# Optimization experiments

Measured on AMD Instinct MI355X. Metric: run time of the kernel, lower is better.

Reference implementation:

```python
import jax, jax.numpy as jnp
import numpy as np

QMIN = 0.0
QMAX = 255.0  # uint8, asymmetric


def fake_quant(x, scale, zp):
    # asymmetric uint8 fake-quantization: q = clamp(round(x/s + zp), 0, 255); dq = (q - zp) * s
    s = scale.reshape(())
    z = zp.reshape(())
    q = jnp.clip(jnp.round(x / s + z), QMIN, QMAX)
    return (q - z) * s


def setup_inputs() -> dict:
    key = jax.random.key(0)
    k1, k2 = jax.random.split(key)
    B, M, K, N = 4, 2048, 4096, 4096
    x1 = jax.random.normal(k1, (B, M, K), dtype=jnp.float32)
    x2 = jax.random.normal(k2, (B, K, N), dtype=jnp.float32)
    # realistic learned per-tensor scale / zero-point for ~N(0,1) data over uint8 range
    x1_scale = jnp.full((1,), 8.0 / 255.0, dtype=jnp.float32)
    x1_zp = jnp.full((1,), 128.0, dtype=jnp.float32)
    x2_scale = jnp.full((1,), 8.0 / 255.0, dtype=jnp.float32)
    x2_zp = jnp.full((1,), 128.0, dtype=jnp.float32)
    return {"x1": x1, "x2": x2, "x1_scale": x1_scale, "x1_zp": x1_zp,
            "x2_scale": x2_scale, "x2_zp": x2_zp}


def reference(x1, x2, x1_scale, x1_zp, x2_scale, x2_zp):
    q1 = fake_quant(x1, x1_scale, x1_zp)  # [B, M, K]
    q2 = fake_quant(x2, x2_scale, x2_zp)  # [B, K, N]
    return jnp.matmul(q1, q2)             # [B, M, N]
```

## Files before the change

### kernel.cpp

```cpp
#include <hip/hip_runtime.h>
#include <stdint.h>

typedef int v4i __attribute__((ext_vector_type(4)));

#define GLOBAL_AS __attribute__((address_space(1)))
#define LDS_AS __attribute__((address_space(3)))

__device__ __forceinline__ int quant1(float x, float s, float z, int zi) {
    float q = rintf(x / s + z);
    q = fminf(fmaxf(q, 0.0f), 255.0f);
    return (int)q - zi;
}

__device__ __forceinline__ unsigned qpack4(float4 v, float s, float z, int zi) {
    unsigned q0 = (unsigned)(quant1(v.x, s, z, zi) & 255);
    unsigned q1 = (unsigned)(quant1(v.y, s, z, zi) & 255);
    unsigned q2 = (unsigned)(quant1(v.z, s, z, zi) & 255);
    unsigned q3 = (unsigned)(quant1(v.w, s, z, zi) & 255);
    return q0 | (q1 << 8) | (q2 << 16) | (q3 << 24);
}

__global__ __launch_bounds__(256) void quant_lin(const float* __restrict__ x,
                                                 int8_t* __restrict__ out,
                                                 const float* __restrict__ sp,
                                                 const float* __restrict__ zp,
                                                 long n16) {
    float s = sp[0], z = zp[0];
    int zi = (int)rintf(z);
    long i = (long)blockIdx.x * 256 + threadIdx.x;
    if (i >= n16) return;
    const float4* xv = (const float4*)x;
    uint4 w;
    w.x = qpack4(xv[i * 4 + 0], s, z, zi);
    w.y = qpack4(xv[i * 4 + 1], s, z, zi);
    w.z = qpack4(xv[i * 4 + 2], s, z, zi);
    w.w = qpack4(xv[i * 4 + 3], s, z, zi);
    ((uint4*)out)[i] = w;
}

__global__ __launch_bounds__(256) void quant_bt(const float* __restrict__ x,
                                                int8_t* __restrict__ out,
                                                const float* __restrict__ sp,
                                                const float* __restrict__ zp) {
    constexpr int K = 4096, N = 4096;
    float s = sp[0], z = zp[0];
    int zi = (int)rintf(z);
    size_t bin = (size_t)blockIdx.z * K * N;
    int tid = threadIdx.x;
    int bk = tid >> 4;
    int bn = tid & 15;
    int k0 = blockIdx.y * 64, n0 = blockIdx.x * 64;
    __shared__ unsigned lds[64][17];
    unsigned o0 = 0, o1 = 0, o2 = 0, o3 = 0;
#pragma unroll
    for (int r = 0; r < 4; ++r) {
        float4 v = *(const float4*)(x + bin + (size_t)(k0 + bk * 4 + r) * N + n0 + bn * 4);
        o0 |= (unsigned)(quant1(v.x, s, z, zi) & 255) << (r * 8);
        o1 |= (unsigned)(quant1(v.y, s, z, zi) & 255) << (r * 8);
        o2 |= (unsigned)(quant1(v.z, s, z, zi) & 255) << (r * 8);
        o3 |= (unsigned)(quant1(v.w, s, z, zi) & 255) << (r * 8);
    }
    lds[bn * 4 + 0][bk] = o0;
    lds[bn * 4 + 1][bk] = o1;
    lds[bn * 4 + 2][bk] = o2;
    lds[bn * 4 + 3][bk] = o3;
    __syncthreads();
    int nl = tid >> 2, ch = tid & 3;
    uint4 w;
    w.x = lds[nl][ch * 4 + 0];
    w.y = lds[nl][ch * 4 + 1];
    w.z = lds[nl][ch * 4 + 2];
    w.w = lds[nl][ch * 4 + 3];
    *(uint4*)(out + bin + (size_t)(n0 + nl) * K + k0 + ch * 16) = w;
}

__global__ __launch_bounds__(512, 2) void gemm_i8(const int8_t* __restrict__ A,
                                                  const int8_t* __restrict__ Bt,
                                                  float* __restrict__ C,
                                                  const float* __restrict__ sp1,
                                                  const float* __restrict__ sp2) {
    constexpr int M = 2048, N = 4096, K = 4096;
    constexpr int BM = 256, BN = 256, BK = 128;
    constexpr int NT = K / BK;
    constexpr int NBN = N / BN;

    extern __shared__ char smem[];

    int b = blockIdx.z;
    const int8_t* Ab = A + (size_t)b * M * K;
    const int8_t* Bb = Bt + (size_t)b * N * K;
    float* Cb = C + (size_t)b * M * N;

    int nwg = gridDim.x;
    int wg = blockIdx.x;
    wg = (wg & 7) * (nwg >> 3) + (wg >> 3);
    int by = wg / NBN, bx = wg % NBN;
    int m0 = by * BM, n0 = bx * BN;

    int tid = threadIdx.x;
    int lane = tid & 63, wid = tid >> 6;
    int wr = wid >> 2, wc = wid & 3;
    int l15 = lane & 15, cb = lane >> 4;

    const int8_t* Abase = Ab + (size_t)m0 * K;
    const int8_t* Bbase = Bb + (size_t)n0 * K;

    int row0 = tid >> 2, cc0 = tid & 3;
    int sw0 = cc0 ^ ((row0 >> 1) & 3);
    const size_t JSTEP = (size_t)128 * K;
    const int8_t* pA0 = Abase + (size_t)row0 * K + sw0 * 16;
    const int8_t* pA1 = pA0 + 64;
    const int8_t* pB0 = Bbase + (size_t)row0 * K + sw0 * 16;
    const int8_t* pB1 = pB0 + 64;
    const unsigned dbase = (unsigned)tid * 16;

    int aoff[8], boff[4];
#pragma unroll
    for (int m = 0; m < 8; ++m) {
        int r = wr * 128 + m * 16 + l15;
        aoff[m] = r * 64 + ((cb ^ ((r >> 1) & 3)) * 16);
    }
#pragma unroll
    for (int n = 0; n < 4; ++n) {
        int r = wc * 64 + n * 16 + l15;
        boff[n] = r * 64 + ((cb ^ ((r >> 1) & 3)) * 16);
    }

    v4i zero = {0, 0, 0, 0};
    v4i acc[8][4];
#pragma unroll
    for (int m = 0; m < 8; ++m)
#pragma unroll
        for (int n = 0; n < 4; ++n) acc[m][n] = zero;

#define ISSUE(p, mat, kh, buf)                                                         \
    {                                                                                  \
        char* dst = smem + ((((buf)*2 + (mat)) * 2 + (kh)) * 16384) + dbase;           \
        __builtin_amdgcn_global_load_lds((const GLOBAL_AS void*)(p),                   \
                                         (LDS_AS void*)dst, 16, 0, 0);                 \
        __builtin_amdgcn_global_load_lds((const GLOBAL_AS void*)((p) + JSTEP),         \
                                         (LDS_AS void*)(dst + 8192), 16, 0, 0);        \
    }

#define HALF(Ar, Br, DOISSUE, NWAIT)                                                   \
    {                                                                                  \
        v4i af[8], bf[4];                                                              \
        _Pragma("unroll") for (int n = 0; n < 4; ++n)                                  \
            bf[n] = *(const v4i*)((Br) + boff[n]);                                     \
        _Pragma("unroll") for (int m = 0; m < 8; ++m)                                  \
            af[m] = *(const v4i*)((Ar) + aoff[m]);                                     \
        DOISSUE;                                                                       \
        __builtin_amdgcn_s_setprio(1);                                                 \
        _Pragma("unroll") for (int m = 0; m < 8; ++m)                                  \
            _Pragma("unroll") for (int n = 0; n < 4; ++n)                              \
                acc[m][n] = __builtin_amdgcn_mfma_i32_16x16x64_i8(af[m], bf[n],        \
                                                                  acc[m][n], 0, 0, 0); \
        __builtin_amdgcn_s_setprio(0);                                                 \
        asm volatile("s_waitcnt lgkmcnt(0)\n\ts_waitcnt vmcnt(" #NWAIT ")" ::: "memory"); \
        __builtin_amdgcn_s_barrier();                                                  \
        asm volatile("" ::: "memory");                                                 \
    }

    ISSUE(pA0, 0, 0, 0);
    ISSUE(pB0, 1, 0, 0);
    ISSUE(pA1, 0, 1, 0);
    ISSUE(pB1, 1, 1, 0);
    asm volatile("s_waitcnt vmcnt(4)" ::: "memory");
    __builtin_amdgcn_s_barrier();
    asm volatile("" ::: "memory");

    for (int jt = 0; jt < NT - 1; ++jt) {
        int buf = jt & 1;
        const char* Ar0 = smem + (buf * 4 + 0) * 16384;
        const char* Ar1 = smem + (buf * 4 + 1) * 16384;
        const char* Br0 = smem + (buf * 4 + 2) * 16384;
        const char* Br1 = smem + (buf * 4 + 3) * 16384;
        pA0 += BK; pA1 += BK; pB0 += BK; pB1 += BK;

        HALF(Ar0, Br0, ISSUE(pA0, 0, 0, buf ^ 1); ISSUE(pB0, 1, 0, buf ^ 1), 4)
        HALF(Ar1, Br1, ISSUE(pA1, 0, 1, buf ^ 1); ISSUE(pB1, 1, 1, buf ^ 1), 4)
    }
    {
        int buf = (NT - 1) & 1;
        const char* Ar0 = smem + (buf * 4 + 0) * 16384;
        const char* Ar1 = smem + (buf * 4 + 1) * 16384;
        const char* Br0 = smem + (buf * 4 + 2) * 16384;
        const char* Br1 = smem + (buf * 4 + 3) * 16384;
        HALF(Ar0, Br0, , 0)
        HALF(Ar1, Br1, , 0)
    }

    float sc = sp1[0] * sp2[0];
    int r0 = cb * 4;
#pragma unroll
    for (int m = 0; m < 8; ++m) {
#pragma unroll
        for (int n = 0; n < 4; ++n) {
            float* p = Cb + (size_t)(m0 + wr * 128 + m * 16 + r0) * N +
                       (n0 + wc * 64 + n * 16 + l15);
#pragma unroll
            for (int r = 0; r < 4; ++r) p[(size_t)r * N] = sc * (float)acc[m][n][r];
        }
    }
#undef ISSUE
#undef HALF
}

extern "C" void kernel_launch(void* const* d_in, const int* in_sizes, int n_in,
                              void* d_out, int out_size, void* d_ws, size_t ws_size,
                              hipStream_t stream) {
    const float* x1 = (const float*)d_in[0];
    const float* x2 = (const float*)d_in[1];
    const float* s1 = (const float*)d_in[2];
    const float* z1 = (const float*)d_in[3];
    const float* s2 = (const float*)d_in[4];
    const float* z2 = (const float*)d_in[5];
    float* out = (float*)d_out;

    const int B = 4, M = 2048, K = 4096, N = 4096;
    const size_t ASZ = (size_t)B * M * K;
    const size_t BSZ = (size_t)B * K * N;
    dim3 blk(256);

    static int lds_attr_set = 0;
    if (!lds_attr_set) {
        (void)hipFuncSetAttribute((const void*)gemm_i8,
                                  hipFuncAttributeMaxDynamicSharedMemorySize, 131072);
        lds_attr_set = 1;
    }

    if (ws_size >= ASZ + BSZ) {
        int8_t* Aq = (int8_t*)d_ws;
        int8_t* Bq = Aq + ASZ;
        long n16 = (long)(ASZ / 16);
        quant_lin<<<dim3((unsigned)(n16 / 256)), blk, 0, stream>>>(x1, Aq, s1, z1, n16);
        quant_bt<<<dim3(N / 64, K / 64, B), blk, 0, stream>>>(x2, Bq, s2, z2);
        gemm_i8<<<dim3((M / 256) * (N / 256), 1, B), dim3(512), 131072, stream>>>(
            Aq, Bq, out, s1, s2);
    } else {
        const size_t AB = (size_t)M * K, BB = (size_t)K * N;
        int8_t* Aq = (int8_t*)d_ws;
        int8_t* Bq = Aq + AB;
        for (int b = 0; b < B; ++b) {
            long n16 = (long)(AB / 16);
            quant_lin<<<dim3((unsigned)(n16 / 256)), blk, 0, stream>>>(x1 + (size_t)b * AB, Aq, s1, z1, n16);
            quant_bt<<<dim3(N / 64, K / 64, 1), blk, 0, stream>>>(x2 + (size_t)b * BB, Bq, s2, z2);
            gemm_i8<<<dim3((M / 256) * (N / 256), 1, 1), dim3(512), 131072, stream>>>(
                Aq, Bq, out + (size_t)b * M * N, s1, s2);
        }
    }
}
```

Measured before the change: 251.5 us.

## Shrink GEMM tile to 256x128x64 with triple-buffered LDS pipeline

```diff
diff --git a/kernel.cpp b/kernel.cpp
--- a/kernel.cpp
+++ b/kernel.cpp
@@ -74,15 +74,16 @@
     *(uint4*)(out + bin + (size_t)(n0 + nl) * K + k0 + ch * 16) = w;
 }
 
-__global__ __launch_bounds__(512, 2) void gemm_i8(const int8_t* __restrict__ A,
+__global__ __launch_bounds__(256, 2) void gemm_i8(const int8_t* __restrict__ A,
                                                   const int8_t* __restrict__ Bt,
                                                   float* __restrict__ C,
                                                   const float* __restrict__ sp1,
                                                   const float* __restrict__ sp2) {
     constexpr int M = 2048, N = 4096, K = 4096;
-    constexpr int BM = 256, BN = 256, BK = 128;
+    constexpr int BM = 256, BN = 128, BK = 64;
     constexpr int NT = K / BK;
     constexpr int NBN = N / BN;
+    constexpr int SLOT = 24576;
 
     extern __shared__ char smem[];
 
@@ -99,19 +100,14 @@
 
     int tid = threadIdx.x;
     int lane = tid & 63, wid = tid >> 6;
-    int wr = wid >> 2, wc = wid & 3;
+    int wr = wid >> 1, wc = wid & 1;
     int l15 = lane & 15, cb = lane >> 4;
-
-    const int8_t* Abase = Ab + (size_t)m0 * K;
-    const int8_t* Bbase = Bb + (size_t)n0 * K;
 
     int row0 = tid >> 2, cc0 = tid & 3;
     int sw0 = cc0 ^ ((row0 >> 1) & 3);
-    const size_t JSTEP = (size_t)128 * K;
-    const int8_t* pA0 = Abase + (size_t)row0 * K + sw0 * 16;
-    const int8_t* pA1 = pA0 + 64;
-    const int8_t* pB0 = Bbase + (size_t)row0 * K + sw0 * 16;
-    const int8_t* pB1 = pB0 + 64;
+    const size_t JSTEP = (size_t)64 * K;
+    const int8_t* pAi = Ab + (size_t)(m0 + row0) * K + sw0 * 16;
+    const int8_t* pBi = Bb + (size_t)(n0 + row0) * K + sw0 * 16;
     const unsigned dbase = (unsigned)tid * 16;
 
     int aoff[8], boff[4];
@@ -123,7 +119,7 @@
 #pragma unroll
     for (int n = 0; n < 4; ++n) {
         int r = wc * 64 + n * 16 + l15;
-        boff[n] = r * 64 + ((cb ^ ((r >> 1) & 3)) * 16);
+        boff[n] = 16384 + r * 64 + ((cb ^ ((r >> 1) & 3)) * 16);
     }
 
     v4i zero = {0, 0, 0, 0};
@@ -133,22 +129,28 @@
 #pragma unroll
         for (int n = 0; n < 4; ++n) acc[m][n] = zero;
 
-#define ISSUE(p, mat, kh, buf)                                                         \
+#define ISSUE(S)                                                                       \
     {                                                                                  \
-        char* dst = smem + ((((buf)*2 + (mat)) * 2 + (kh)) * 16384) + dbase;           \
-        __builtin_amdgcn_global_load_lds((const GLOBAL_AS void*)(p),                   \
-                                         (LDS_AS void*)dst, 16, 0, 0);                 \
-        __builtin_amdgcn_global_load_lds((const GLOBAL_AS void*)((p) + JSTEP),         \
-                                         (LDS_AS void*)(dst + 8192), 16, 0, 0);        \
-    }
-
-#define HALF(Ar, Br, DOISSUE, NWAIT)                                                   \
+        char* da = smem + (S)*SLOT + dbase;                                            \
+        _Pragma("unroll") for (int j = 0; j < 4; ++j)                                  \
+            __builtin_amdgcn_global_load_lds((const GLOBAL_AS void*)(pAi + j * JSTEP), \
+                                             (LDS_AS void*)(da + j * 4096), 16, 0, 0); \
+        char* db = smem + (S)*SLOT + 16384 + dbase;                                    \
+        _Pragma("unroll") for (int j = 0; j < 2; ++j)                                  \
+            __builtin_amdgcn_global_load_lds((const GLOBAL_AS void*)(pBi + j * JSTEP), \
+                                             (LDS_AS void*)(db + j * 4096), 16, 0, 0); \
+        pAi += BK;                                                                     \
+        pBi += BK;                                                                     \
+    }
+
+#define TILE(S, DOISSUE, DOWAIT)                                                       \
     {                                                                                  \
+        const char* Ar = smem + (S)*SLOT;                                              \
         v4i af[8], bf[4];                                                              \
         _Pragma("unroll") for (int n = 0; n < 4; ++n)                                  \
-            bf[n] = *(const v4i*)((Br) + boff[n]);                                     \
+            bf[n] = *(const v4i*)(Ar + boff[n]);                                       \
         _Pragma("unroll") for (int m = 0; m < 8; ++m)                                  \
-            af[m] = *(const v4i*)((Ar) + aoff[m]);                                     \
+            af[m] = *(const v4i*)(Ar + aoff[m]);                                       \
         DOISSUE;                                                                       \
         __builtin_amdgcn_s_setprio(1);                                                 \
         _Pragma("unroll") for (int m = 0; m < 8; ++m)                                  \
@@ -156,39 +158,33 @@
                 acc[m][n] = __builtin_amdgcn_mfma_i32_16x16x64_i8(af[m], bf[n],        \
                                                                   acc[m][n], 0, 0, 0); \
         __builtin_amdgcn_s_setprio(0);                                                 \
-        asm volatile("s_waitcnt lgkmcnt(0)\n\ts_waitcnt vmcnt(" #NWAIT ")" ::: "memory"); \
-        __builtin_amdgcn_s_barrier();                                                  \
-        asm volatile("" ::: "memory");                                                 \
-    }
-
-    ISSUE(pA0, 0, 0, 0);
-    ISSUE(pB0, 1, 0, 0);
-    ISSUE(pA1, 0, 1, 0);
-    ISSUE(pB1, 1, 1, 0);
-    asm volatile("s_waitcnt vmcnt(4)" ::: "memory");
+        DOWAIT;                                                                        \
+    }
+
+#define W6                                                                             \
+    asm volatile("s_waitcnt lgkmcnt(0)\n\ts_waitcnt vmcnt(6)" ::: "memory");           \
+    __builtin_amdgcn_s_barrier();                                                      \
+    asm volatile("" ::: "memory");
+#define W0                                                                             \
+    asm volatile("s_waitcnt lgkmcnt(0)\n\ts_waitcnt vmcnt(0)" ::: "memory");           \
+    __builtin_amdgcn_s_barrier();                                                      \
+    asm volatile("" ::: "memory");
+
+    ISSUE(0);
+    ISSUE(1);
+    asm volatile("s_waitcnt vmcnt(6)" ::: "memory");
     __builtin_amdgcn_s_barrier();
     asm volatile("" ::: "memory");
 
-    for (int jt = 0; jt < NT - 1; ++jt) {
-        int buf = jt & 1;
-        const char* Ar0 = smem + (buf * 4 + 0) * 16384;
-        const char* Ar1 = smem + (buf * 4 + 1) * 16384;
-        const char* Br0 = smem + (buf * 4 + 2) * 16384;
-        const char* Br1 = smem + (buf * 4 + 3) * 16384;
-        pA0 += BK; pA1 += BK; pB0 += BK; pB1 += BK;
-
-        HALF(Ar0, Br0, ISSUE(pA0, 0, 0, buf ^ 1); ISSUE(pB0, 1, 0, buf ^ 1), 4)
-        HALF(Ar1, Br1, ISSUE(pA1, 0, 1, buf ^ 1); ISSUE(pB1, 1, 1, buf ^ 1), 4)
-    }
-    {
-        int buf = (NT - 1) & 1;
-        const char* Ar0 = smem + (buf * 4 + 0) * 16384;
-        const char* Ar1 = smem + (buf * 4 + 1) * 16384;
-        const char* Br0 = smem + (buf * 4 + 2) * 16384;
-        const char* Br1 = smem + (buf * 4 + 3) * 16384;
-        HALF(Ar0, Br0, , 0)
-        HALF(Ar1, Br1, , 0)
-    }
+    for (int tt = 0; tt < 60; tt += 3) {
+        TILE(0, ISSUE(2), W6)
+        TILE(1, ISSUE(0), W6)
+        TILE(2, ISSUE(1), W6)
+    }
+    TILE(0, ISSUE(2), W6)
+    TILE(1, ISSUE(0), W6)
+    TILE(2, , W0)
+    TILE(0, , )
 
     float sc = sp1[0] * sp2[0];
     int r0 = cb * 4;
@@ -203,7 +199,9 @@
         }
     }
 #undef ISSUE
-#undef HALF
+#undef TILE
+#undef W6
+#undef W0
 }
 
 extern "C" void kernel_launch(void* const* d_in, const int* in_sizes, int n_in,
@@ -225,7 +223,7 @@
     static int lds_attr_set = 0;
     if (!lds_attr_set) {
         (void)hipFuncSetAttribute((const void*)gemm_i8,
-                                  hipFuncAttributeMaxDynamicSharedMemorySize, 131072);
+                                  hipFuncAttributeMaxDynamicSharedMemorySize, 73728);
         lds_attr_set = 1;
     }
 
@@ -235,7 +233,7 @@
         long n16 = (long)(ASZ / 16);
         quant_lin<<<dim3((unsigned)(n16 / 256)), blk, 0, stream>>>(x1, Aq, s1, z1, n16);
         quant_bt<<<dim3(N / 64, K / 64, B), blk, 0, stream>>>(x2, Bq, s2, z2);
-        gemm_i8<<<dim3((M / 256) * (N / 256), 1, B), dim3(512), 131072, stream>>>(
+        gemm_i8<<<dim3((M / 256) * (N / 128), 1, B), dim3(256), 73728, stream>>>(
             Aq, Bq, out, s1, s2);
     } else {
         const size_t AB = (size_t)M * K, BB = (size_t)K * N;
@@ -245,7 +243,7 @@
             long n16 = (long)(AB / 16);
             quant_lin<<<dim3((unsigned)(n16 / 256)), blk, 0, stream>>>(x1 + (size_t)b * AB, Aq, s1, z1, n16);
             quant_bt<<<dim3(N / 64, K / 64, 1), blk, 0, stream>>>(x2 + (size_t)b * BB, Bq, s2, z2);
-            gemm_i8<<<dim3((M / 256) * (N / 256), 1, 1), dim3(512), 131072, stream>>>(
+            gemm_i8<<<dim3((M / 256) * (N / 128), 1, 1), dim3(256), 73728, stream>>>(
                 Aq, Bq, out + (size_t)b * M * N, s1, s2);
         }
     }
```

Result: slower. 262.4 us (+4.3%).
